# Kernel optimization log

Hardware: AMD Instinct MI355X
Metric: run time of the kernel (lower is better)

## Reference

```python
import jax, jax.numpy as jnp
import numpy as np

DIM = 1024
HEADS = 16
EPS = 1e-05
B, T, C, H, W = 2, 16, DIM, 32, 32


def setup_inputs() -> dict:
    key = jax.random.key(0)
    ks = jax.random.split(key, 4)
    s = 1.0 / np.sqrt(DIM)
    return {
        "x": jax.random.normal(ks[0], (B, T, C, H, W), dtype=jnp.float32),
        "ln_w": jnp.ones((C,), dtype=jnp.float32),
        "ln_b": jnp.zeros((C,), dtype=jnp.float32),
        "Wq": jax.random.normal(ks[1], (C, C), dtype=jnp.float32) * s,
        "Wk": jax.random.normal(ks[2], (C, C), dtype=jnp.float32) * s,
        "Wv": jax.random.normal(ks[3], (C, C), dtype=jnp.float32) * s,
    }


def reference(x, ln_w, ln_b, Wq, Wk, Wv):
    b, t, c, h, w = x.shape
    heads = HEADS
    dh = c // heads
    scale = dh ** (-0.5)

    # Channel LayerNorm: normalize over C per (b,t,h,w)
    xc = jnp.transpose(x, (0, 1, 3, 4, 2))  # [B,T,H,W,C]
    mu = jnp.mean(xc, axis=-1, keepdims=True)
    var = jnp.mean(jnp.square(xc - mu), axis=-1, keepdims=True)
    xn = (xc - mu) * jax.lax.rsqrt(var + EPS) * ln_w + ln_b  # [B,T,H,W,C]

    # Q/K from spatial mean-pool
    pooled = jnp.mean(xn, axis=(2, 3))  # [B,T,C]
    q = pooled @ Wq.T  # [B,T,C]
    k = pooled @ Wk.T  # [B,T,C]

    # V per pixel; torch permutes to [B,W,H,T,C] then flattens W-major
    v = jnp.transpose(xn, (0, 3, 2, 1, 4)).reshape(b, h * w, t, c)  # [B,HW(w-major),T,C]
    v = v @ Wv.T

    q = q.reshape(b, t, heads, dh).transpose(0, 2, 1, 3) * scale  # [B,h,T,dh]
    k = k.reshape(b, t, heads, dh).transpose(0, 2, 3, 1)          # [B,h,dh,T]
    v = v.reshape(b, h * w, t, heads, dh).transpose(0, 1, 3, 2, 4)  # [B,HW,h,T,dh]

    attn = jax.nn.softmax(jnp.matmul(q, k), axis=-1)  # [B,h,T,T]
    out = jnp.einsum('bhst,bnhtd->bnhsd', attn, v)    # [B,HW,h,T,dh]
    # permute(0,3,2,4,1) -> [B,T,h,dh,HW], then view as (H,W)
    out = out.transpose(0, 3, 2, 4, 1).reshape(b, t, c, h, w)
    return out
```

## Files before the change

### kernel.cpp

```cpp
#include <hip/hip_runtime.h>
#include <stdint.h>
#include <stddef.h>

#define CDIM 1024
#define HWD  1024
#define TD   16
#define BD   2
#define NH   16
#define DHD  64

typedef __attribute__((ext_vector_type(8))) short bf16x8;
typedef __attribute__((ext_vector_type(4))) short bf16x4;
typedef __attribute__((ext_vector_type(4))) float f32x4;

static __device__ __forceinline__ short f2bf(float f) {
  uint32_t u = __builtin_bit_cast(uint32_t, f);
  uint32_t r = (u + 0x7FFFu + ((u >> 16) & 1u)) >> 16;
  return (short)(uint16_t)r;
}
static __device__ __forceinline__ float bf2f(short s) {
  return __builtin_bit_cast(float, (uint32_t)((uint16_t)s) << 16);
}

static __device__ __forceinline__ void gl_lds16(const short* g, short* l) {
  __builtin_amdgcn_global_load_lds((const __attribute__((address_space(1))) unsigned int*)g,
                                   (__attribute__((address_space(3))) unsigned int*)l,
                                   16, 0, 0);
}

__global__ void k_cast_w(const float* __restrict__ W, short* __restrict__ Wb) {
  int i = (blockIdx.x * 256 + threadIdx.x) * 4;
  f32x4 v = *(const f32x4*)&W[i];
  Wb[i + 0] = f2bf(v[0]);
  Wb[i + 1] = f2bf(v[1]);
  Wb[i + 2] = f2bf(v[2]);
  Wb[i + 3] = f2bf(v[3]);
}

__global__ void k_ln_t(const float* __restrict__ x, const float* __restrict__ lnw,
                       const float* __restrict__ lnb, short* __restrict__ xnT) {
  int bt = blockIdx.y;
  int p0 = blockIdx.x * 64;
  int tid = threadIdx.x;
  int pl = tid & 63;
  int cq = tid >> 6;
  const float* xs = x + (size_t)bt * CDIM * HWD;

  float s = 0.f, s2 = 0.f;
  for (int c = cq * 256; c < cq * 256 + 256; ++c) {
    float v = xs[(size_t)c * HWD + p0 + pl];
    s += v; s2 += v * v;
  }
  __shared__ float red[8][64];
  red[cq][pl] = s;
  red[4 + cq][pl] = s2;
  __syncthreads();
  float st  = red[0][pl] + red[1][pl] + red[2][pl] + red[3][pl];
  float st2 = red[4][pl] + red[5][pl] + red[6][pl] + red[7][pl];
  float mu   = st * (1.0f / CDIM);
  float var  = st2 * (1.0f / CDIM) - mu * mu;
  float rstd = rsqrtf(var + 1e-5f);

  __shared__ short tile[64 * 68];
  short* outB = xnT + (size_t)bt * CDIM * HWD;

  for (int cb = 0; cb < 16; ++cb) {
    #pragma unroll
    for (int cc2 = 0; cc2 < 16; ++cc2) {
      int c = cb * 64 + cq * 16 + cc2;
      float v = xs[(size_t)c * HWD + p0 + pl];
      float xn = (v - mu) * rstd * lnw[c] + lnb[c];
      tile[pl * 68 + cq * 16 + cc2] = f2bf(xn);
    }
    __syncthreads();
    #pragma unroll
    for (int it = 0; it < 2; ++it) {
      int ch = it * 256 + tid;
      int plo = ch >> 3;
      int c8 = (ch & 7) * 8;
      bf16x4 a = *(const bf16x4*)&tile[plo * 68 + c8];
      bf16x4 b = *(const bf16x4*)&tile[plo * 68 + c8 + 4];
      int pq = p0 + plo;
      int q = (pq & 31) * 32 + (pq >> 5);
      short* dst = outB + (size_t)q * CDIM + cb * 64 + c8;
      *(bf16x4*)dst = a;
      *(bf16x4*)(dst + 4) = b;
    }
    __syncthreads();
  }
}

__global__ void k_pool_part(const short* __restrict__ xnT, float* __restrict__ part) {
  int bt = blockIdx.y, pc = blockIdx.x;
  int c8 = threadIdx.x * 8;
  const short* base = xnT + (size_t)bt * CDIM * HWD;
  float s[8] = {};
  for (int p = pc * 128; p < pc * 128 + 128; ++p) {
    bf16x8 v = *(const bf16x8*)&base[(size_t)p * CDIM + c8];
    #pragma unroll
    for (int k = 0; k < 8; ++k) s[k] += bf2f(v[k]);
  }
  float* pr = part + ((size_t)pc * BD * TD + bt) * CDIM + c8;
  #pragma unroll
  for (int k = 0; k < 8; ++k) pr[k] = s[k];
}
__global__ void k_pool_red(const float* __restrict__ part, float* __restrict__ pooled,
                           short* __restrict__ pooledb) {
  int bt = blockIdx.y;
  int c = blockIdx.x * 256 + threadIdx.x;
  float s = 0.f;
  #pragma unroll
  for (int pc = 0; pc < 8; ++pc) s += part[((size_t)pc * BD * TD + bt) * CDIM + c];
  float m = s * (1.0f / HWD);
  pooled[bt * CDIM + c] = m;
  pooledb[bt * CDIM + c] = f2bf(m);
}

__global__ __launch_bounds__(256) void k_qk_mfma(const short* __restrict__ Wqkb,
                                                 const short* __restrict__ pooledb,
                                                 float* __restrict__ qm,
                                                 float* __restrict__ km) {
  int n0 = blockIdx.x * 128;
  __shared__ __align__(16) short lA[32 * 32];
  __shared__ __align__(16) short lB[128 * 32];
  int tid = threadIdx.x, lane = tid & 63, wid = tid >> 6;
  int s0 = wid * 128 + lane, s1 = s0 + 64;
  int fr = lane & 15, fk = (lane >> 4) * 8;
  f32x4 acc[2][2] = {};

  for (int kt = 0; kt < CDIM / 32; ++kt) {
    int k0 = kt * 32;
    __syncthreads();
    gl_lds16(&Wqkb[(size_t)(n0 + (s0 >> 2)) * CDIM + k0 + (s0 & 3) * 8], &lB[s0 * 8]);
    gl_lds16(&Wqkb[(size_t)(n0 + (s1 >> 2)) * CDIM + k0 + (s1 & 3) * 8], &lB[s1 * 8]);
    if (wid < 2) {
      gl_lds16(&pooledb[(size_t)(tid >> 2) * CDIM + k0 + (tid & 3) * 8], &lA[tid * 8]);
    }
    __syncthreads();
    bf16x8 af[2], bfr[2];
    #pragma unroll
    for (int mi = 0; mi < 2; ++mi)
      af[mi] = *(const bf16x8*)&lA[(mi * 16 + fr) * 32 + fk];
    #pragma unroll
    for (int ni = 0; ni < 2; ++ni)
      bfr[ni] = *(const bf16x8*)&lB[(wid * 32 + ni * 16 + fr) * 32 + fk];
    #pragma unroll
    for (int mi = 0; mi < 2; ++mi)
      #pragma unroll
      for (int ni = 0; ni < 2; ++ni)
        acc[mi][ni] = __builtin_amdgcn_mfma_f32_16x16x32_bf16(af[mi], bfr[ni], acc[mi][ni], 0, 0, 0);
  }

  int cr = lane >> 4;
  #pragma unroll
  for (int mi = 0; mi < 2; ++mi)
    #pragma unroll
    for (int ni = 0; ni < 2; ++ni)
      #pragma unroll
      for (int rr = 0; rr < 4; ++rr) {
        int row = mi * 16 + cr * 4 + rr;
        int col = n0 + wid * 32 + ni * 16 + fr;
        float v = acc[mi][ni][rr];
        if (col < 1024) qm[(size_t)row * CDIM + col] = v;
        else            km[(size_t)row * CDIM + col - 1024] = v;
      }
}

__global__ void k_attn(const float* __restrict__ qm, const float* __restrict__ km,
                       float* __restrict__ attn) {
  int bg = blockIdx.x;
  int b = bg >> 4, g = bg & 15;
  int s = threadIdx.x >> 4, t = threadIdx.x & 15;
  const float* qr = qm + (size_t)(b * TD + s) * CDIM + g * DHD;
  const float* kr = km + (size_t)(b * TD + t) * CDIM + g * DHD;
  float d = 0.f;
  #pragma unroll
  for (int i = 0; i < DHD; ++i) d += qr[i] * kr[i];
  d *= 0.125f;
  float m = d;
  #pragma unroll
  for (int off = 8; off; off >>= 1) m = fmaxf(m, __shfl_xor(m, off, 16));
  float e = __expf(d - m);
  float sum = e;
  #pragma unroll
  for (int off = 8; off; off >>= 1) sum += __shfl_xor(sum, off, 16);
  attn[(size_t)bg * 256 + s * 16 + t] = e / sum;
}

__global__ __launch_bounds__(256) void k_vgemm(const short* __restrict__ Wb,
                                               const short* __restrict__ xnT,
                                               short* __restrict__ vp) {
  int bt = blockIdx.z;
  int m0 = blockIdx.y * 128;
  int n0 = blockIdx.x * 128;
  const short* A = Wb;
  const short* Bm = xnT + (size_t)bt * CDIM * HWD;
  __shared__ __align__(16) short lA[128 * 32];
  __shared__ __align__(16) short lB[128 * 32];
  int tid = threadIdx.x;
  int lane = tid & 63;
  int wid = tid >> 6;
  int wr = (wid >> 1) * 64;
  int wc = (wid & 1) * 64;
  f32x4 acc[4][4] = {};

  int sm = tid >> 2, sk = (tid & 3) * 8;
  const short* gA = A + (size_t)(m0 + sm) * CDIM + sk;
  const short* gB = Bm + (size_t)(n0 + sm) * CDIM + sk;
  short* dA = &lA[tid * 8];
  short* dB = &lB[tid * 8];
  int fr = lane & 15, fk = (lane >> 4) * 8;

  for (int kt = 0; kt < CDIM / 32; ++kt) {
    __syncthreads();
    gl_lds16(gA + kt * 32, dA);
    gl_lds16(gA + kt * 32 + (size_t)64 * CDIM, dA + 64 * 32);
    gl_lds16(gB + kt * 32, dB);
    gl_lds16(gB + kt * 32 + (size_t)64 * CDIM, dB + 64 * 32);
    __syncthreads();
    bf16x8 af[4], bfr[4];
    #pragma unroll
    for (int mi = 0; mi < 4; ++mi)
      af[mi] = *(const bf16x8*)&lA[(wr + mi * 16 + fr) * 32 + fk];
    #pragma unroll
    for (int ni = 0; ni < 4; ++ni)
      bfr[ni] = *(const bf16x8*)&lB[(wc + ni * 16 + fr) * 32 + fk];
    #pragma unroll
    for (int mi = 0; mi < 4; ++mi)
      #pragma unroll
      for (int ni = 0; ni < 4; ++ni)
        acc[mi][ni] = __builtin_amdgcn_mfma_f32_16x16x32_bf16(af[mi], bfr[ni], acc[mi][ni], 0, 0, 0);
  }

  short* outB = vp + (size_t)bt * CDIM * HWD;
  int cr = lane >> 4;
  #pragma unroll
  for (int mi = 0; mi < 4; ++mi)
    #pragma unroll
    for (int ni = 0; ni < 4; ++ni)
      #pragma unroll
      for (int r = 0; r < 4; ++r) {
        int row = m0 + wr + mi * 16 + cr * 4 + r;
        int col = n0 + wc + ni * 16 + fr;
        outB[(size_t)row * HWD + col] = f2bf(acc[mi][ni][r]);
      }
}

__global__ __launch_bounds__(256) void k_mix(const short* __restrict__ vp,
                                             const float* __restrict__ attn,
                                             float* __restrict__ out) {
  int c = blockIdx.x;
  int b = blockIdx.y;
  int g = c >> 6;
  __shared__ __align__(16) short vpl[TD * HWD];
  __shared__ float at[256];
  int tid = threadIdx.x;
  at[tid] = attn[(size_t)(b * NH + g) * 256 + tid];
  #pragma unroll
  for (int j = 0; j < 8; ++j) {
    int chunk = j * 256 + tid;
    int t = chunk >> 7, qc = chunk & 127;
    bf16x8 v = *(const bf16x8*)&vp[((size_t)(b * TD + t) * CDIM + c) * HWD + qc * 8];
    *(bf16x8*)&vpl[t * HWD + qc * 8] = v;
  }
  __syncthreads();
  int p = tid * 4;
  #pragma unroll
  for (int sh = 0; sh < 2; ++sh) {
    f32x4 acc[8] = {};
    #pragma unroll
    for (int t = 0; t < TD; ++t) {
      bf16x4 v4 = *(const bf16x4*)&vpl[t * HWD + p];
      f32x4 vf = {bf2f(v4[0]), bf2f(v4[1]), bf2f(v4[2]), bf2f(v4[3])};
      #pragma unroll
      for (int s8 = 0; s8 < 8; ++s8) {
        float a = at[(sh * 8 + s8) * 16 + t];
        acc[s8] += a * vf;
      }
    }
    #pragma unroll
    for (int s8 = 0; s8 < 8; ++s8) {
      int s = sh * 8 + s8;
      *(f32x4*)&out[((size_t)(b * TD + s) * CDIM + c) * HWD + p] = acc[s8];
    }
  }
}

extern "C" void kernel_launch(void* const* d_in, const int* in_sizes, int n_in,
                              void* d_out, int out_size, void* d_ws, size_t ws_size,
                              hipStream_t stream) {
  const float* x   = (const float*)d_in[0];
  const float* lnw = (const float*)d_in[1];
  const float* lnb = (const float*)d_in[2];
  const float* Wq  = (const float*)d_in[3];
  const float* Wk  = (const float*)d_in[4];
  const float* Wv  = (const float*)d_in[5];
  float* out = (float*)d_out;

  char* ws = (char*)d_ws;
  const size_t XNT_OFF   = 0;
  const size_t VP_OFF    = XNT_OFF + 67108864;
  const size_t WB_OFF    = VP_OFF + 67108864;
  const size_t WQKB_OFF  = WB_OFF + 2097152;
  const size_t POOLP_OFF = WQKB_OFF + 4194304;
  const size_t POOL_OFF  = POOLP_OFF + 1048576;
  const size_t POOLB_OFF = POOL_OFF + 131072;
  const size_t QM_OFF    = POOLB_OFF + 65536;
  const size_t KM_OFF    = QM_OFF + 131072;
  const size_t ATTN_OFF  = KM_OFF + 131072;

  short* xnT    = (short*)(ws + XNT_OFF);
  short* vp     = (short*)(ws + VP_OFF);
  short* Wb     = (short*)(ws + WB_OFF);
  short* Wqkb   = (short*)(ws + WQKB_OFF);
  float* poolp  = (float*)(ws + POOLP_OFF);
  float* pooled = (float*)(ws + POOL_OFF);
  short* poolb  = (short*)(ws + POOLB_OFF);
  float* qm     = (float*)(ws + QM_OFF);
  float* km     = (float*)(ws + KM_OFF);
  float* attn   = (float*)(ws + ATTN_OFF);

  k_cast_w<<<dim3(1024), 256, 0, stream>>>(Wv, Wb);
  k_cast_w<<<dim3(1024), 256, 0, stream>>>(Wq, Wqkb);
  k_cast_w<<<dim3(1024), 256, 0, stream>>>(Wk, Wqkb + 1048576);
  k_ln_t<<<dim3(16, 32), 256, 0, stream>>>(x, lnw, lnb, xnT);
  k_pool_part<<<dim3(8, 32), 128, 0, stream>>>(xnT, poolp);
  k_pool_red<<<dim3(4, 32), 256, 0, stream>>>(poolp, pooled, poolb);
  k_qk_mfma<<<dim3(16), 256, 0, stream>>>(Wqkb, poolb, qm, km);
  k_attn<<<dim3(32), 256, 0, stream>>>(qm, km, attn);
  k_vgemm<<<dim3(8, 8, 32), 256, 0, stream>>>(Wb, xnT, vp);
  k_mix<<<dim3(1024, 2), 256, 0, stream>>>(vp, attn, out);
}
```

Measured before the change: 238.3 us.

## Rewrite V GEMM with 256x256 tiles, double-buffered LDS, swizzle, and interleaved prefetch

```diff
diff --git a/kernel.cpp b/kernel.cpp
--- a/kernel.cpp
+++ b/kernel.cpp
@@ -187,61 +187,121 @@
   attn[(size_t)bg * 256 + s * 16 + t] = e / sum;
 }
 
-__global__ __launch_bounds__(256) void k_vgemm(const short* __restrict__ Wb,
-                                               const short* __restrict__ xnT,
-                                               short* __restrict__ vp) {
-  int bt = blockIdx.z;
-  int m0 = blockIdx.y * 128;
-  int n0 = blockIdx.x * 128;
-  const short* A = Wb;
+__global__ __launch_bounds__(512, 2) void k_vgemm(const short* __restrict__ Wb,
+                                                  const short* __restrict__ xnT,
+                                                  short* __restrict__ vp) {
+  int bid = blockIdx.x;
+  int swz = (bid & 7) * 64 + (bid >> 3);
+  int bt = swz >> 4;
+  int m0 = ((swz >> 2) & 3) * 256;
+  int n0 = (swz & 3) * 256;
   const short* Bm = xnT + (size_t)bt * CDIM * HWD;
-  __shared__ __align__(16) short lA[128 * 32];
-  __shared__ __align__(16) short lB[128 * 32];
-  int tid = threadIdx.x;
-  int lane = tid & 63;
-  int wid = tid >> 6;
-  int wr = (wid >> 1) * 64;
-  int wc = (wid & 1) * 64;
-  f32x4 acc[4][4] = {};
-
-  int sm = tid >> 2, sk = (tid & 3) * 8;
-  const short* gA = A + (size_t)(m0 + sm) * CDIM + sk;
-  const short* gB = Bm + (size_t)(n0 + sm) * CDIM + sk;
-  short* dA = &lA[tid * 8];
-  short* dB = &lB[tid * 8];
-  int fr = lane & 15, fk = (lane >> 4) * 8;
-
-  for (int kt = 0; kt < CDIM / 32; ++kt) {
-    __syncthreads();
-    gl_lds16(gA + kt * 32, dA);
-    gl_lds16(gA + kt * 32 + (size_t)64 * CDIM, dA + 64 * 32);
-    gl_lds16(gB + kt * 32, dB);
-    gl_lds16(gB + kt * 32 + (size_t)64 * CDIM, dB + 64 * 32);
-    __syncthreads();
-    bf16x8 af[4], bfr[4];
+
+  __shared__ __align__(16) short lA[2][256 * 64];
+  __shared__ __align__(16) short lB[2][256 * 64];
+
+  int tid = threadIdx.x, lane = tid & 63, wid = tid >> 6;
+  int wm = wid >> 2, wn = wid & 3;
+
+  int srow = wid * 8 + (lane >> 3);
+  int schunk = (lane & 7) ^ (lane >> 3);
+  const short* gA = Wb + (size_t)(m0 + srow) * CDIM + schunk * 8;
+  const short* gB = Bm + (size_t)(n0 + srow) * CDIM + schunk * 8;
+  int doff = wid * 512 + lane * 8;
+
+  int fr = lane & 15, klane = lane >> 4;
+  int c0 = ((klane ^ (fr & 7)) * 8);
+  int rA = (wm * 128 + fr) * 64;
+  int rB = (wn * 64 + fr) * 64;
+
+  f32x4 acc[8][4] = {};
+  bf16x8 bq[4], af[4];
+
+#define ISSUE(p, kt1, nb)                                                      \
+  do {                                                                         \
+    gl_lds16(gA + (size_t)(p) * 64 * CDIM + (kt1) * 64, &lA[nb][(p) * 4096 + doff]); \
+    gl_lds16(gB + (size_t)(p) * 64 * CDIM + (kt1) * 64, &lB[nb][(p) * 4096 + doff]); \
+  } while (0)
+#define RDA(mi, ks, b) (*(const bf16x8*)&lA[b][rA + (mi) * 1024 + (c0 ^ ((ks) * 32))])
+#define RDB(ni, ks, b) (*(const bf16x8*)&lB[b][rB + (ni) * 1024 + (c0 ^ ((ks) * 32))])
+
+  ISSUE(0, 0, 0); ISSUE(1, 0, 0); ISSUE(2, 0, 0); ISSUE(3, 0, 0);
+
+  for (int kt = 0; kt < 16; ++kt) {
+    int cur = kt & 1, nxt = cur ^ 1;
+    bool st = (kt + 1 < 16);
+    if (st) {
+      ISSUE(0, kt + 1, nxt);
+      asm volatile("s_waitcnt vmcnt(2)" ::: "memory");
+    } else {
+      asm volatile("s_waitcnt vmcnt(0)" ::: "memory");
+    }
+    __builtin_amdgcn_s_barrier();
+    #pragma unroll
+    for (int ni = 0; ni < 4; ++ni) bq[ni] = RDB(ni, 0, cur);
+    #pragma unroll
+    for (int mi = 0; mi < 4; ++mi) af[mi] = RDA(mi, 0, cur);
+    __builtin_amdgcn_s_setprio(1);
     #pragma unroll
     for (int mi = 0; mi < 4; ++mi)
-      af[mi] = *(const bf16x8*)&lA[(wr + mi * 16 + fr) * 32 + fk];
-    #pragma unroll
-    for (int ni = 0; ni < 4; ++ni)
-      bfr[ni] = *(const bf16x8*)&lB[(wc + ni * 16 + fr) * 32 + fk];
+      #pragma unroll
+      for (int ni = 0; ni < 4; ++ni)
+        acc[mi][ni] = __builtin_amdgcn_mfma_f32_16x16x32_bf16(af[mi], bq[ni], acc[mi][ni], 0, 0, 0);
+    __builtin_amdgcn_s_setprio(0);
+    __builtin_amdgcn_s_barrier();
+    #pragma unroll
+    for (int mi = 0; mi < 4; ++mi) af[mi] = RDA(4 + mi, 0, cur);
+    if (st) ISSUE(1, kt + 1, nxt);
+    __builtin_amdgcn_s_barrier();
+    __builtin_amdgcn_s_setprio(1);
     #pragma unroll
     for (int mi = 0; mi < 4; ++mi)
       #pragma unroll
       for (int ni = 0; ni < 4; ++ni)
-        acc[mi][ni] = __builtin_amdgcn_mfma_f32_16x16x32_bf16(af[mi], bfr[ni], acc[mi][ni], 0, 0, 0);
-  }
+        acc[4 + mi][ni] = __builtin_amdgcn_mfma_f32_16x16x32_bf16(af[mi], bq[ni], acc[4 + mi][ni], 0, 0, 0);
+    __builtin_amdgcn_s_setprio(0);
+    __builtin_amdgcn_s_barrier();
+    #pragma unroll
+    for (int ni = 0; ni < 4; ++ni) bq[ni] = RDB(ni, 1, cur);
+    #pragma unroll
+    for (int mi = 0; mi < 4; ++mi) af[mi] = RDA(mi, 1, cur);
+    if (st) ISSUE(2, kt + 1, nxt);
+    __builtin_amdgcn_s_barrier();
+    __builtin_amdgcn_s_setprio(1);
+    #pragma unroll
+    for (int mi = 0; mi < 4; ++mi)
+      #pragma unroll
+      for (int ni = 0; ni < 4; ++ni)
+        acc[mi][ni] = __builtin_amdgcn_mfma_f32_16x16x32_bf16(af[mi], bq[ni], acc[mi][ni], 0, 0, 0);
+    __builtin_amdgcn_s_setprio(0);
+    __builtin_amdgcn_s_barrier();
+    #pragma unroll
+    for (int mi = 0; mi < 4; ++mi) af[mi] = RDA(4 + mi, 1, cur);
+    if (st) ISSUE(3, kt + 1, nxt);
+    __builtin_amdgcn_s_barrier();
+    __builtin_amdgcn_s_setprio(1);
+    #pragma unroll
+    for (int mi = 0; mi < 4; ++mi)
+      #pragma unroll
+      for (int ni = 0; ni < 4; ++ni)
+        acc[4 + mi][ni] = __builtin_amdgcn_mfma_f32_16x16x32_bf16(af[mi], bq[ni], acc[4 + mi][ni], 0, 0, 0);
+    __builtin_amdgcn_s_setprio(0);
+    __builtin_amdgcn_s_barrier();
+  }
+#undef ISSUE
+#undef RDA
+#undef RDB
 
   short* outB = vp + (size_t)bt * CDIM * HWD;
   int cr = lane >> 4;
   #pragma unroll
-  for (int mi = 0; mi < 4; ++mi)
+  for (int mi = 0; mi < 8; ++mi)
     #pragma unroll
     for (int ni = 0; ni < 4; ++ni)
       #pragma unroll
       for (int r = 0; r < 4; ++r) {
-        int row = m0 + wr + mi * 16 + cr * 4 + r;
-        int col = n0 + wc + ni * 16 + fr;
+        int row = m0 + wm * 128 + mi * 16 + cr * 4 + r;
+        int col = n0 + wn * 64 + ni * 16 + fr;
         outB[(size_t)row * HWD + col] = f2bf(acc[mi][ni][r]);
       }
 }
@@ -328,6 +388,6 @@
   k_pool_red<<<dim3(4, 32), 256, 0, stream>>>(poolp, pooled, poolb);
   k_qk_mfma<<<dim3(16), 256, 0, stream>>>(Wqkb, poolb, qm, km);
   k_attn<<<dim3(32), 256, 0, stream>>>(qm, km, attn);
-  k_vgemm<<<dim3(8, 8, 32), 256, 0, stream>>>(Wb, xnT, vp);
+  k_vgemm<<<dim3(512), 512, 0, stream>>>(Wb, xnT, vp);
   k_mix<<<dim3(1024, 2), 256, 0, stream>>>(vp, attn, out);
 }
```

Result: faster. 226.6 us (-4.9%).
